# Performance work log

Measured on AMD Instinct MI355X. Metric: run time of the kernel, lower is better.

## Reference

```python
import jax, jax.numpy as jnp
import numpy as np
import math

IMG_SIZE = 768
NUM_CLASSES = 90
THRESHOLD = 0.05
IOU_THRESHOLD = 0.5
MAX_DETECTIONS = 100
K_CAND = 512  # per-class candidate pool before greedy NMS
RATIOS = [(1.0, 1.0), (1.4, 0.7), (0.7, 1.4)]
SCALES = [2 ** 0, 2 ** (1.0 / 3.0), 2 ** (2.0 / 3.0)]


def _generate_anchors():
    anchor_scale = 4.0
    pyramid_levels = [3, 4, 5, 6, 7]
    all_levels = []
    for lv in pyramid_levels:
        stride = 2 ** lv
        size = anchor_scale * 2 ** lv
        grid = IMG_SIZE // stride
        sx = np.arange(grid) * stride
        sy, sx = np.meshgrid(np.arange(grid) * stride, sx, indexing='ij')
        # torch meshgrid(shift_y, shift_x, indexing='ij') -> rows are y
        yy, xx = np.meshgrid(np.arange(grid) * stride, np.arange(grid) * stride, indexing='ij')
        shifts = np.stack([xx.ravel(), yy.ravel(), xx.ravel(), yy.ravel()], axis=1).astype(np.float32)
        base = []
        for r in RATIOS:
            for s in SCALES:
                w = size * s * math.sqrt(r[0] / r[1])
                h = size * s * math.sqrt(r[1] / r[0])
                base.append([-w / 2, -h / 2, w / 2, h / 2])
        base = np.asarray(base, dtype=np.float32)  # [9,4]
        anc = (base[None, :, :] + shifts[:, None, :]).reshape(-1, 4)
        all_levels.append(anc)
    return np.concatenate(all_levels, axis=0)  # [110484,4]


def setup_inputs() -> dict:
    key = jax.random.key(0)
    k1, k2, k3 = jax.random.split(key, 3)
    A = 110484
    x = jax.random.normal(k1, (1, 3, IMG_SIZE, IMG_SIZE), dtype=jnp.float32)
    regression = jax.random.normal(k2, (1, A, 4), dtype=jnp.float32) * 0.3
    classification = jax.random.normal(k3, (1, A, NUM_CLASSES), dtype=jnp.float32) - 2.0
    anchors = jnp.asarray(_generate_anchors())
    return {"x": x, "regression": regression, "classification": classification, "anchors": anchors}


def _decode_and_clip(anchors, deltas, H, W):
    # BBoxTransform (RetinaNet-style): deltas = (dx, dy, dw, dh)
    wa = anchors[:, 2] - anchors[:, 0]
    ha = anchors[:, 3] - anchors[:, 1]
    cxa = anchors[:, 0] + 0.5 * wa
    cya = anchors[:, 1] + 0.5 * ha
    dx, dy, dw, dh = deltas[:, 0], deltas[:, 1], deltas[:, 2], deltas[:, 3]
    cx = cxa + dx * wa
    cy = cya + dy * ha
    w = jnp.exp(dw) * wa
    h = jnp.exp(dh) * ha
    x1 = jnp.clip(cx - 0.5 * w, 0.0, W)
    y1 = jnp.clip(cy - 0.5 * h, 0.0, H)
    x2 = jnp.clip(cx + 0.5 * w, 0.0, W)
    y2 = jnp.clip(cy + 0.5 * h, 0.0, H)
    return jnp.stack([x1, y1, x2, y2], axis=1)  # [A,4]


def _pairwise_iou(b):  # [K,4] -> [K,K]
    area = (b[:, 2] - b[:, 0]) * (b[:, 3] - b[:, 1])
    xx1 = jnp.maximum(b[:, None, 0], b[None, :, 0])
    yy1 = jnp.maximum(b[:, None, 1], b[None, :, 1])
    xx2 = jnp.minimum(b[:, None, 2], b[None, :, 2])
    yy2 = jnp.minimum(b[:, None, 3], b[None, :, 3])
    inter = jnp.clip(xx2 - xx1, 0.0) * jnp.clip(yy2 - yy1, 0.0)
    return inter / (area[:, None] + area[None, :] - inter + 1e-8)


def _greedy_nms(iou_c, valid_c):
    # boxes are pre-sorted by descending score; fixed-iteration greedy NMS
    def step(suppressed, i):
        keep_i = valid_c[i] & jnp.logical_not(suppressed[i])
        suppressed = jnp.where(keep_i, suppressed | (iou_c[i] > IOU_THRESHOLD), suppressed)
        return suppressed, keep_i
    _, keep = jax.lax.scan(step, jnp.zeros(iou_c.shape[0], dtype=bool), jnp.arange(iou_c.shape[0]))
    return keep  # [K]


def _postprocess(x, regression, classification, anchors):
    H, W = x.shape[2], x.shape[3]
    boxes = _decode_and_clip(anchors, regression[0], float(H), float(W))  # [A,4]
    scores = jax.nn.sigmoid(classification[0])                            # [A,C]
    # per-class top-K candidate pool (sorted desc), fixed-shape NMS
    vals, idx = jax.lax.top_k(scores.T, K_CAND)        # [C,K]
    cand = boxes[idx]                                   # [C,K,4]
    valid = vals > THRESHOLD                            # [C,K]
    iou = jax.vmap(_pairwise_iou)(cand)                 # [C,K,K]
    keep = jax.vmap(_greedy_nms)(iou, valid)            # [C,K]
    kept_scores = jnp.where(keep, vals, -1.0).reshape(-1)  # [C*K]
    top_vals, flat_idx = jax.lax.top_k(kept_scores, MAX_DETECTIONS)
    labels = (flat_idx // K_CAND).astype(jnp.float32)
    det_boxes = cand.reshape(-1, 4)[flat_idx]
    ok = top_vals > 0.0
    det = jnp.concatenate([
        jnp.zeros((MAX_DETECTIONS, 1), dtype=jnp.float32),  # batch ids (batch=1 -> 0)
        det_boxes,
        top_vals[:, None],
        labels[:, None],
    ], axis=1)  # [100,7]
    return jnp.where(ok[:, None], det, 0.0)


def reference(x, regression, classification, anchors):
    return _postprocess(x, regression, classification, anchors)
```

## Files before the change

kernel.cpp:

```cpp
#include <hip/hip_runtime.h>
#include <math.h>


#define A_N   110484
#define C_N   90
#define KCAND 512
#define NBINS 8192
#define KSH   19
#define MAXDET 100
#define IMG_F 768.0f
#define THRESH 0.05f
#define NS    4
#define VTOT  (A_N / 4)
#define VS4   ((VTOT + NS - 1) / NS)
#define SL_CAP 1024
#define CAND_N (NS * KCAND)
#define KEEP_CAP 100
#define T_BLKS ((A_N + 63) / 64)
#define S_BLKS (C_N * NS)
#define D_BLKS ((A_N + 255) / 256)
#define FCAP  512

typedef unsigned int u32;
typedef unsigned long long u64;

__device__ __forceinline__ u32 fkey(float f) {
    u32 u = __float_as_uint(f);
    return (u & 0x80000000u) ? ~u : (u | 0x80000000u);
}
__device__ __forceinline__ float unfkey(u32 k) {
    u32 u = (k & 0x80000000u) ? (k ^ 0x80000000u) : ~k;
    return __uint_as_float(u);
}
__device__ __forceinline__ u64 shflx64(u64 v, int m) {
    u32 lo = (u32)__shfl_xor((int)(u32)v, m, 64);
    u32 hi = (u32)__shfl_xor((int)(v >> 32), m, 64);
    return ((u64)hi << 32) | lo;
}

__global__ __launch_bounds__(256)
void prep_kernel(const float* __restrict__ cls,
                 u32* __restrict__ keysT) {
    __shared__ u32 tile[64 * 91];
    const int a0 = blockIdx.x * 64;
    const int lim = min(64, A_N - a0);
    const int n4 = (lim * C_N) >> 2;
    const float4* src4 = (const float4*)(cls + (size_t)a0 * C_N);
    for (int i4 = threadIdx.x; i4 < n4; i4 += 256) {
        float4 x4 = src4[i4];
        const u32 base = (u32)(4 * i4);
        float xs[4] = { x4.x, x4.y, x4.z, x4.w };
        #pragma unroll
        for (int k = 0; k < 4; ++k) {
            u32 i = base + k;
            u32 aa = i / C_N, c = i % C_N;
            float s = 1.0f / (1.0f + expf(-xs[k]));
            tile[aa * 91 + c] = fkey(s);
        }
    }
    __syncthreads();
    for (int j = threadIdx.x; j < C_N * 64; j += 256) {
        int c = j >> 6, aa = j & 63;
        if (aa < lim)
            keysT[(size_t)c * A_N + a0 + aa] = tile[aa * 91 + c];
    }
}

__global__ __launch_bounds__(256)
void select_kernel(const u32* __restrict__ keysT,
                   const float* __restrict__ anchors,
                   const float* __restrict__ reg,
                   float4* __restrict__ boxes,
                   u64* __restrict__ candbuf) {
    __shared__ u32 hist[NBINS];
    __shared__ u32 csum[256];
    __shared__ u64 lbuf[SL_CAP];
    __shared__ u32 sPv;
    __shared__ int lcnt;
    const int tid = threadIdx.x;

    if (blockIdx.x >= S_BLKS) {
        int a = (blockIdx.x - S_BLKS) * 256 + tid;
        if (a < A_N) {
            float4 an = ((const float4*)anchors)[a];
            float4 dl = ((const float4*)reg)[a];
            float wa = an.z - an.x, ha = an.w - an.y;
            float cx = an.x + 0.5f * wa + dl.x * wa;
            float cy = an.y + 0.5f * ha + dl.y * ha;
            float w = expf(dl.z) * wa;
            float h = expf(dl.w) * ha;
            float4 o;
            o.x = fminf(fmaxf(cx - 0.5f * w, 0.0f), IMG_F);
            o.y = fminf(fmaxf(cy - 0.5f * h, 0.0f), IMG_F);
            o.z = fminf(fmaxf(cx + 0.5f * w, 0.0f), IMG_F);
            o.w = fminf(fmaxf(cy + 0.5f * h, 0.0f), IMG_F);
            boxes[a] = o;
        }
        return;
    }
    const int c = blockIdx.x >> 2, s = blockIdx.x & 3;
    const int lo = s * VS4, hiEnd = min(VTOT, lo + VS4);
    const uint4* kv = (const uint4*)(keysT + (size_t)c * A_N);

    for (int i = tid; i < NBINS; i += 256) hist[i] = 0;
    if (tid == 0) { sPv = 0; lcnt = 0; }
    __syncthreads();
    for (int i = lo + tid; i < hiEnd; i += 256) {
        uint4 k = kv[i];
        atomicAdd(&hist[k.x >> KSH], 1u);
        atomicAdd(&hist[k.y >> KSH], 1u);
        atomicAdd(&hist[k.z >> KSH], 1u);
        atomicAdd(&hist[k.w >> KSH], 1u);
    }
    __syncthreads();
    u32 own = 0; const int hi = NBINS - 1 - 32 * tid;
    #pragma unroll 4
    for (int j = 0; j < 32; ++j) own += hist[hi - j];
    csum[tid] = own;
    __syncthreads();
    for (int off = 1; off < 256; off <<= 1) {
        u32 v = csum[tid];
        u32 a = (tid >= off) ? csum[tid - off] : 0u;
        __syncthreads();
        csum[tid] = v + a;
        __syncthreads();
    }
    const u32 incl = csum[tid], excl = incl - own;
    if (excl < (u32)KCAND && incl >= (u32)KCAND) {
        u32 cum = excl;
        for (int j = 0; j < 32; ++j) {
            u32 hv = hist[hi - j];
            if (cum + hv >= (u32)KCAND) { sPv = (u32)(hi - j); break; }
            cum += hv;
        }
    }
    __syncthreads();
    const u32 P = sPv;
    for (int i = lo + tid; i < hiEnd; i += 256) {
        uint4 k = kv[i];
        u32 base = (u32)(4 * i);
        if ((k.x >> KSH) >= P) {
            int p = atomicAdd(&lcnt, 1);
            if (p < SL_CAP) lbuf[p] = (((u64)(~k.x)) << 32) | base;
        }
        if ((k.y >> KSH) >= P) {
            int p = atomicAdd(&lcnt, 1);
            if (p < SL_CAP) lbuf[p] = (((u64)(~k.y)) << 32) | (base + 1);
        }
        if ((k.z >> KSH) >= P) {
            int p = atomicAdd(&lcnt, 1);
            if (p < SL_CAP) lbuf[p] = (((u64)(~k.z)) << 32) | (base + 2);
        }
        if ((k.w >> KSH) >= P) {
            int p = atomicAdd(&lcnt, 1);
            if (p < SL_CAP) lbuf[p] = (((u64)(~k.w)) << 32) | (base + 3);
        }
    }
    __syncthreads();
    const int n = min(lcnt, SL_CAP);
    for (int i = tid; i < SL_CAP; i += 256) if (i >= n) lbuf[i] = ~0ULL;
    __syncthreads();

    {
        const int l = tid & 63, w = tid >> 6;
        int ii[4]; u64 v[4];
        #pragma unroll
        for (int r = 0; r < 4; ++r) { ii[r] = 256 * w + 64 * r + l; v[r] = lbuf[ii[r]]; }
        __syncthreads();
        #pragma unroll
        for (u32 kk = 2; kk <= 1024; kk <<= 1) {
            #pragma unroll
            for (u32 j = kk >> 1; j > 0; j >>= 1) {
                if (j >= 256) {
                    #pragma unroll
                    for (int r = 0; r < 4; ++r) lbuf[ii[r]] = v[r];
                    __syncthreads();
                    #pragma unroll
                    for (int r = 0; r < 4; ++r) {
                        u64 pv = lbuf[ii[r] ^ j];
                        bool up = ((ii[r] & kk) == 0);
                        bool m = (((ii[r] & j) == 0) == up);
                        v[r] = m ? (v[r] < pv ? v[r] : pv) : (v[r] > pv ? v[r] : pv);
                    }
                    __syncthreads();
                } else if (j >= 64) {
                    const int rx = (int)(j >> 6);
                    u64 nv[4];
                    #pragma unroll
                    for (int r = 0; r < 4; ++r) {
                        u64 pv = v[r ^ rx];
                        bool up = ((ii[r] & kk) == 0);
                        bool m = (((ii[r] & j) == 0) == up);
                        nv[r] = m ? (v[r] < pv ? v[r] : pv) : (v[r] > pv ? v[r] : pv);
                    }
                    #pragma unroll
                    for (int r = 0; r < 4; ++r) v[r] = nv[r];
                } else {
                    #pragma unroll
                    for (int r = 0; r < 4; ++r) {
                        u64 pv = shflx64(v[r], (int)j);
                        bool up = ((ii[r] & kk) == 0);
                        bool m = (((ii[r] & j) == 0) == up);
                        v[r] = m ? (v[r] < pv ? v[r] : pv) : (v[r] > pv ? v[r] : pv);
                    }
                }
            }
        }
        u64* cb = candbuf + (size_t)c * CAND_N + (size_t)s * KCAND;
        const bool rev = (s & 1);
        #pragma unroll
        for (int r = 0; r < 4; ++r) {
            if (ii[r] < KCAND) {
                int d = rev ? (KCAND - 1 - ii[r]) : ii[r];
                cb[d] = v[r];
            }
        }
    }
}

__global__ __launch_bounds__(1024)
void snms_kernel(const u64* __restrict__ candbuf,
                 const float4* __restrict__ boxes,
                 u32* __restrict__ keptbuf, u32* __restrict__ cnt2) {
    __shared__ u64 sortbuf[2][CAND_N];
    __shared__ float bxx[KCAND], byy[KCAND], bzz[KCAND], bww[KCAND];
    __shared__ float ar[KCAND], sc[KCAND];
    __shared__ u32 keepf[16], wbase[17];
    u32* bmask = (u32*)&sortbuf[0][0];
    const int c = blockIdx.x, tid = threadIdx.x;
    const int l = tid & 63, w = tid >> 6;
    const int i0 = 128 * w + l, i1 = i0 + 64;

    const u64* cb = candbuf + (size_t)c * CAND_N;
    u64 v0 = cb[i0], v1 = cb[i1];
    int p = 0;
    #pragma unroll
    for (u32 kk = 1024; kk <= (u32)CAND_N; kk <<= 1) {
        #pragma unroll
        for (u32 j = kk >> 1; j > 0; j >>= 1) {
            if (j >= 128) {
                sortbuf[p][i0] = v0; sortbuf[p][i1] = v1;
                __syncthreads();
                u64 w0 = sortbuf[p][i0 ^ j], w1 = sortbuf[p][i1 ^ j];
                bool m0 = (((i0 & j) == 0) == ((i0 & kk) == 0));
                bool m1 = (((i1 & j) == 0) == ((i1 & kk) == 0));
                v0 = m0 ? (v0 < w0 ? v0 : w0) : (v0 > w0 ? v0 : w0);
                v1 = m1 ? (v1 < w1 ? v1 : w1) : (v1 > w1 ? v1 : w1);
                p ^= 1;
            } else if (j == 64) {
                bool up = ((i0 & kk) == 0);
                u64 mn = v0 < v1 ? v0 : v1, mx = v0 < v1 ? v1 : v0;
                v0 = up ? mn : mx; v1 = up ? mx : mn;
            } else {
                u64 w0 = shflx64(v0, (int)j), w1 = shflx64(v1, (int)j);
                bool m0 = (((i0 & j) == 0) == ((i0 & kk) == 0));
                bool m1 = (((i1 & j) == 0) == ((i1 & kk) == 0));
                v0 = m0 ? (v0 < w0 ? v0 : w0) : (v0 > w0 ? v0 : w0);
                v1 = m1 ? (v1 < w1 ? v1 : w1) : (v1 > w1 ? v1 : w1);
            }
        }
    }
    __syncthreads();

    if (w < 4) {
        u32 idx0 = (u32)v0, key0 = ~((u32)(v0 >> 32));
        u32 idx1 = (u32)v1, key1 = ~((u32)(v1 >> 32));
        sc[i0] = unfkey(key0); sc[i1] = unfkey(key1);
        float4 b0 = boxes[idx0], b1 = boxes[idx1];
        bxx[i0] = b0.x; byy[i0] = b0.y; bzz[i0] = b0.z; bww[i0] = b0.w;
        bxx[i1] = b1.x; byy[i1] = b1.y; bzz[i1] = b1.z; bww[i1] = b1.w;
        ar[i0] = (b0.z - b0.x) * (b0.w - b0.y);
        ar[i1] = (b1.z - b1.x) * (b1.w - b1.y);
    }
    for (int i = tid; i < KCAND * 16; i += 1024) bmask[i] = 0;
    if (tid < 16) keepf[tid] = 0;
    __syncthreads();

    {
        const int i = tid & (KCAND - 1);
        const int half = tid >> 9;
        const int count = (KCAND - 1) - i;
        const int j0 = i + 1 + (half ? (count >> 1) : 0);
        const int j1 = half ? KCAND : (i + 1 + (count >> 1));
        const float bix = bxx[i], biy = byy[i], biz = bzz[i], biw = bww[i];
        const float ai = ar[i];
        u32 m[16];
        #pragma unroll
        for (int q = 0; q < 16; ++q) m[q] = 0;
        for (int j = j0; j < j1; ++j) {
            float xx1 = fmaxf(bix, bxx[j]), yy1 = fmaxf(biy, byy[j]);
            float xx2 = fminf(biz, bzz[j]), yy2 = fminf(biw, bww[j]);
            float inter = fmaxf(xx2 - xx1, 0.0f) * fmaxf(yy2 - yy1, 0.0f);
            float uni = ai + ar[j] - inter + 1e-8f;
            if (inter > 0.5f * uni) m[j >> 5] |= (1u << (j & 31));
        }
        #pragma unroll
        for (int q = 0; q < 16; ++q)
            if (m[q]) atomicOr(&bmask[i * 16 + q], m[q]);
    }
    __syncthreads();

    if (tid < 64) {
        const int lw = tid & 15;
        u32 removed = 0, keepw = 0;
        u32 rA[8], rB[8]; float sA[8], sB[8];
        #pragma unroll
        for (int k = 0; k < 8; ++k) { rA[k] = bmask[k * 16 + lw]; sA[k] = sc[k]; }
        #pragma unroll 1
        for (int ch = 0; ch < 64; ch += 2) {
            const int tb1 = (ch + 1) * 8;
            #pragma unroll
            for (int k = 0; k < 8; ++k) { rB[k] = bmask[(tb1 + k) * 16 + lw]; sB[k] = sc[tb1 + k]; }
            {
                const int tb = ch * 8;
                #pragma unroll
                for (int k = 0; k < 8; ++k) {
                    const int t = tb + k;
                    u32 rw = (u32)__builtin_amdgcn_readlane((int)removed, t >> 5);
                    bool d = (sA[k] > THRESH) && (((rw >> (t & 31)) & 1u) == 0u);
                    removed |= d ? rA[k] : 0u;
                    keepw |= (d && (tid == (t >> 5))) ? (1u << (t & 31)) : 0u;
                }
            }
            const int tb2 = (ch + 2 < 64) ? (ch + 2) * 8 : 0;
            #pragma unroll
            for (int k = 0; k < 8; ++k) { rA[k] = bmask[(tb2 + k) * 16 + lw]; sA[k] = sc[tb2 + k]; }
            {
                #pragma unroll
                for (int k = 0; k < 8; ++k) {
                    const int t = tb1 + k;
                    u32 rw = (u32)__builtin_amdgcn_readlane((int)removed, t >> 5);
                    bool d = (sB[k] > THRESH) && (((rw >> (t & 31)) & 1u) == 0u);
                    removed |= d ? rB[k] : 0u;
                    keepw |= (d && (tid == (t >> 5))) ? (1u << (t & 31)) : 0u;
                }
            }
        }
        if (tid < 16) keepf[tid] = keepw;
    }
    __syncthreads();

    if (tid == 0) {
        u32 t = 0;
        for (int q = 0; q < 16; ++q) { wbase[q] = t; t += __popc(keepf[q]); }
        wbase[16] = t;
        cnt2[c] = (t < (u32)KEEP_CAP) ? t : (u32)KEEP_CAP;
    }
    __syncthreads();
    if (tid < KCAND) {
        u32 word = keepf[tid >> 5];
        u32 bit = (u32)tid & 31u;
        if ((word >> bit) & 1u) {
            u32 rank = wbase[tid >> 5] + __popc(word & ((1u << bit) - 1u));
            if (rank < (u32)KEEP_CAP) {
                float s = sc[tid];
                uint4 a, b;
                a.x = ~fkey(s);
                a.y = (u32)(c * KCAND + tid);
                a.z = __float_as_uint(bxx[tid]);
                a.w = __float_as_uint(byy[tid]);
                b.x = __float_as_uint(bzz[tid]);
                b.y = __float_as_uint(bww[tid]);
                b.z = __float_as_uint(s);
                b.w = 0u;
                uint4* e = (uint4*)(keptbuf + ((size_t)c * KEEP_CAP + rank) * 8);
                e[0] = a; e[1] = b;
            }
        }
    }
}

__global__ __launch_bounds__(1024)
void final_kernel(const u32* __restrict__ keptbuf, const u32* __restrict__ cnt2,
                  float* __restrict__ out) {
    __shared__ u32 hist[NBINS];
    __shared__ u32 csum[1024];
    __shared__ u64 ebuf[FCAP];
    __shared__ u32 eidx[FCAP];
    __shared__ u32 scnt[C_N];
    __shared__ u32 sP;
    __shared__ int sN;
    const int tid = threadIdx.x;
    const int TOT = C_N * KEEP_CAP;

    for (int i = tid; i < MAXDET * 7; i += 1024) out[i] = 0.0f;
    for (int i = tid; i < NBINS; i += 1024) hist[i] = 0;
    if (tid < C_N) scnt[tid] = cnt2[tid];
    if (tid == 0) { sN = 0; sP = NBINS - 1; }
    __syncthreads();

    for (int i = tid; i < TOT; i += 1024) {
        u32 c = (u32)i / KEEP_CAP, pp = (u32)i % KEEP_CAP;
        if (pp < scnt[c]) {
            u32 khi = keptbuf[(size_t)i * 8];
            atomicAdd(&hist[khi >> KSH], 1u);
        }
    }
    __syncthreads();
    u32 own = 0; const int lo = 8 * tid;
    #pragma unroll
    for (int j = 0; j < 8; ++j) own += hist[lo + j];
    csum[tid] = own;
    __syncthreads();
    for (int off = 1; off < 1024; off <<= 1) {
        u32 v = csum[tid];
        u32 a = (tid >= off) ? csum[tid - off] : 0u;
        __syncthreads();
        csum[tid] = v + a;
        __syncthreads();
    }
    const u32 incl = csum[tid], excl = incl - own;
    if (excl < (u32)MAXDET && incl >= (u32)MAXDET) {
        u32 cum = excl;
        for (int j = 0; j < 8; ++j) {
            u32 h = hist[lo + j];
            if (cum + h >= (u32)MAXDET) { sP = (u32)(lo + j); break; }
            cum += h;
        }
    }
    __syncthreads();
    const u32 P = sP;
    for (int i = tid; i < TOT; i += 1024) {
        u32 c = (u32)i / KEEP_CAP, pp = (u32)i % KEEP_CAP;
        if (pp < scnt[c]) {
            const uint2 v2 = *((const uint2*)(keptbuf + (size_t)i * 8));
            if ((v2.x >> KSH) <= P) {
                int p = atomicAdd(&sN, 1);
                if (p < FCAP) {
                    ebuf[p] = ((u64)v2.x << 32) | v2.y;
                    eidx[p] = (u32)i;
                }
            }
        }
    }
    __syncthreads();
    const int n = min(sN, FCAP);
    u32 m = 128; while ((int)m < n) m <<= 1;
    for (int i = tid; i < (int)m; i += 1024) if (i >= n) ebuf[i] = ~0ULL;
    __syncthreads();
    for (u32 kk = 2; kk <= m; kk <<= 1) {
        for (u32 j = kk >> 1; j > 0; j >>= 1) {
            u32 i = (u32)tid;
            if (i < m) {
                u32 ixj = i ^ j;
                if (ixj > i) {
                    u64 x = ebuf[i], y = ebuf[ixj];
                    bool up = ((i & kk) == 0);
                    if (up ? (x > y) : (x < y)) {
                        ebuf[i] = y; ebuf[ixj] = x;
                        u32 t = eidx[i]; eidx[i] = eidx[ixj]; eidx[ixj] = t;
                    }
                }
            }
            __syncthreads();
        }
    }
    if (tid < MAXDET && tid < n) {
        u64 comp = ebuf[tid];
        if (comp != ~0ULL) {
            const uint4* e = (const uint4*)(keptbuf + (size_t)eidx[tid] * 8);
            uint4 a = e[0], b = e[1];
            float* o = out + tid * 7;
            o[0] = 0.0f;
            o[1] = __uint_as_float(a.z); o[2] = __uint_as_float(a.w);
            o[3] = __uint_as_float(b.x); o[4] = __uint_as_float(b.y);
            o[5] = __uint_as_float(b.z);
            o[6] = (float)(((u32)comp) >> 9);
        }
    }
}

extern "C" void kernel_launch(void* const* d_in, const int* in_sizes, int n_in,
                              void* d_out, int out_size, void* d_ws, size_t ws_size,
                              hipStream_t stream) {
    const float* reg     = (const float*)d_in[1];
    const float* cls     = (const float*)d_in[2];
    const float* anchors = (const float*)d_in[3];
    float* out = (float*)d_out;

    char* ws = (char*)d_ws;
    size_t off = 0;
    auto alloc = [&](size_t bytes) -> void* {
        void* p = ws + off;
        off = (off + bytes + 255) & ~(size_t)255;
        return p;
    };
    u32*    keysT   = (u32*)   alloc((size_t)C_N * A_N * sizeof(u32));
    float4* boxes   = (float4*)alloc((size_t)A_N * sizeof(float4));
    u64*    candbuf = (u64*)   alloc((size_t)C_N * CAND_N * sizeof(u64));
    u32*    keptbuf = (u32*)   alloc((size_t)C_N * KEEP_CAP * 8 * sizeof(u32));
    u32*    cnt2    = (u32*)   alloc((size_t)C_N * sizeof(u32));
    (void)ws_size;

    prep_kernel<<<T_BLKS, 256, 0, stream>>>(cls, keysT);
    select_kernel<<<S_BLKS + D_BLKS, 256, 0, stream>>>(keysT, anchors, reg, boxes, candbuf);
    snms_kernel<<<C_N, 1024, 0, stream>>>(candbuf, boxes, keptbuf, cnt2);
    final_kernel<<<1, 1024, 0, stream>>>(keptbuf, cnt2, out);
}
```

Measured before the change: 216.9 us.

## Widen prep tile, drop bmask atomics, pair greedy NMS steps

Raises the anchors-per-block in the transpose/sigmoid prep kernel from 64 to 128. In the IoU mask build, the split between the two halves now falls on a 32-bit word boundary, so each half writes its own mask words with plain stores. This removes the zeroing pass and the atomicOr calls. The serial greedy NMS loop now resolves two candidates per step, using a readlane of the mask row to check whether the first suppresses the second. This halves the serial dependency chain at the cost of slightly more logic per step.

```diff
diff --git a/kernel.cpp b/kernel.cpp
--- a/kernel.cpp
+++ b/kernel.cpp
@@ -16,7 +16,8 @@
 #define SL_CAP 1024
 #define CAND_N (NS * KCAND)
 #define KEEP_CAP 100
-#define T_BLKS ((A_N + 63) / 64)
+#define TILE_A 128
+#define T_BLKS ((A_N + TILE_A - 1) / TILE_A)
 #define S_BLKS (C_N * NS)
 #define D_BLKS ((A_N + 255) / 256)
 #define FCAP  512
@@ -41,9 +42,9 @@
 __global__ __launch_bounds__(256)
 void prep_kernel(const float* __restrict__ cls,
                  u32* __restrict__ keysT) {
-    __shared__ u32 tile[64 * 91];
-    const int a0 = blockIdx.x * 64;
-    const int lim = min(64, A_N - a0);
+    __shared__ u32 tile[TILE_A * 91];
+    const int a0 = blockIdx.x * TILE_A;
+    const int lim = min(TILE_A, A_N - a0);
     const int n4 = (lim * C_N) >> 2;
     const float4* src4 = (const float4*)(cls + (size_t)a0 * C_N);
     for (int i4 = threadIdx.x; i4 < n4; i4 += 256) {
@@ -59,8 +60,8 @@
         }
     }
     __syncthreads();
-    for (int j = threadIdx.x; j < C_N * 64; j += 256) {
-        int c = j >> 6, aa = j & 63;
+    for (int j = threadIdx.x; j < C_N * TILE_A; j += 256) {
+        int c = j >> 7, aa = j & (TILE_A - 1);
         if (aa < lim)
             keysT[(size_t)c * A_N + a0 + aa] = tile[aa * 91 + c];
     }
@@ -272,7 +273,6 @@
         ar[i0] = (b0.z - b0.x) * (b0.w - b0.y);
         ar[i1] = (b1.z - b1.x) * (b1.w - b1.y);
     }
-    for (int i = tid; i < KCAND * 16; i += 1024) bmask[i] = 0;
     if (tid < 16) keepf[tid] = 0;
     __syncthreads();
 
@@ -280,8 +280,11 @@
         const int i = tid & (KCAND - 1);
         const int half = tid >> 9;
         const int count = (KCAND - 1) - i;
-        const int j0 = i + 1 + (half ? (count >> 1) : 0);
-        const int j1 = half ? KCAND : (i + 1 + (count >> 1));
+        int mid = (i + 1 + (count >> 1) + 31) & ~31;
+        if (mid > KCAND) mid = KCAND;
+        const int j0 = half ? mid : (i + 1);
+        const int j1 = half ? KCAND : mid;
+        const int wsplit = mid >> 5;
         const float bix = bxx[i], biy = byy[i], biz = bzz[i], biw = bww[i];
         const float ai = ar[i];
         u32 m[16];
@@ -294,9 +297,9 @@
             float uni = ai + ar[j] - inter + 1e-8f;
             if (inter > 0.5f * uni) m[j >> 5] |= (1u << (j & 31));
         }
-        #pragma unroll
-        for (int q = 0; q < 16; ++q)
-            if (m[q]) atomicOr(&bmask[i * 16 + q], m[q]);
+        const int qlo = half ? wsplit : 0;
+        const int qhi = half ? 16 : wsplit;
+        for (int q = qlo; q < qhi; ++q) bmask[i * 16 + q] = m[q];
     }
     __syncthreads();
 
@@ -314,12 +317,17 @@
             {
                 const int tb = ch * 8;
                 #pragma unroll
-                for (int k = 0; k < 8; ++k) {
+                for (int k = 0; k < 8; k += 2) {
                     const int t = tb + k;
-                    u32 rw = (u32)__builtin_amdgcn_readlane((int)removed, t >> 5);
-                    bool d = (sA[k] > THRESH) && (((rw >> (t & 31)) & 1u) == 0u);
-                    removed |= d ? rA[k] : 0u;
-                    keepw |= (d && (tid == (t >> 5))) ? (1u << (t & 31)) : 0u;
+                    u32 rw   = (u32)__builtin_amdgcn_readlane((int)removed, t >> 5);
+                    u32 mrow = (u32)__builtin_amdgcn_readlane((int)rA[k],   t >> 5);
+                    bool d0 = (sA[k] > THRESH) && (((rw >> (t & 31)) & 1u) == 0u);
+                    const u32 b1 = (u32)(t + 1) & 31u;
+                    bool d1 = (sA[k + 1] > THRESH) && (((rw >> b1) & 1u) == 0u)
+                              && !(d0 && ((mrow >> b1) & 1u));
+                    removed |= (d0 ? rA[k] : 0u) | (d1 ? rA[k + 1] : 0u);
+                    if (tid == (t >> 5))
+                        keepw |= (d0 ? (1u << (t & 31)) : 0u) | (d1 ? (1u << b1) : 0u);
                 }
             }
             const int tb2 = (ch + 2 < 64) ? (ch + 2) * 8 : 0;
@@ -327,12 +335,17 @@
             for (int k = 0; k < 8; ++k) { rA[k] = bmask[(tb2 + k) * 16 + lw]; sA[k] = sc[tb2 + k]; }
             {
                 #pragma unroll
-                for (int k = 0; k < 8; ++k) {
+                for (int k = 0; k < 8; k += 2) {
                     const int t = tb1 + k;
-                    u32 rw = (u32)__builtin_amdgcn_readlane((int)removed, t >> 5);
-                    bool d = (sB[k] > THRESH) && (((rw >> (t & 31)) & 1u) == 0u);
-                    removed |= d ? rB[k] : 0u;
-                    keepw |= (d && (tid == (t >> 5))) ? (1u << (t & 31)) : 0u;
+                    u32 rw   = (u32)__builtin_amdgcn_readlane((int)removed, t >> 5);
+                    u32 mrow = (u32)__builtin_amdgcn_readlane((int)rB[k],   t >> 5);
+                    bool d0 = (sB[k] > THRESH) && (((rw >> (t & 31)) & 1u) == 0u);
+                    const u32 b1 = (u32)(t + 1) & 31u;
+                    bool d1 = (sB[k + 1] > THRESH) && (((rw >> b1) & 1u) == 0u)
+                              && !(d0 && ((mrow >> b1) & 1u));
+                    removed |= (d0 ? rB[k] : 0u) | (d1 ? rB[k + 1] : 0u);
+                    if (tid == (t >> 5))
+                        keepw |= (d0 ? (1u << (t & 31)) : 0u) | (d1 ? (1u << b1) : 0u);
                 }
             }
         }
```

Result: slower. 232.8 us (+7.3%).
